# Kernel tuning notes

Hardware: AMD Instinct MI355X
Metric: run time of the kernel (lower is better)

## Reference

```python
import jax, jax.numpy as jnp
import numpy as np

NUM_CLASSES = 19

def setup_inputs() -> dict:
    key = jax.random.key(0)
    k1, k2 = jax.random.split(key)
    feats = jax.random.normal(k1, (8, 256, 128, 256), dtype=jnp.float32)
    y_down = jax.random.randint(k2, (8, 128, 256), 0, NUM_CLASSES, dtype=jnp.int64)
    return {"feats": feats, "y_down": y_down}

def reference(feats, y_down):
    # feats: [B, C, H, W]; y_down: [B, H, W] int labels in [0, NUM_CLASSES)
    B, C, H, W = feats.shape
    x = jnp.transpose(feats, (0, 2, 3, 1)).reshape(-1, C)   # [N, C], N = B*H*W
    seg = y_down.reshape(-1).astype(jnp.int32)              # [N]
    # per-class sum of feature vectors and pixel counts (fused segment reduce)
    sums = jax.ops.segment_sum(x, seg, num_segments=NUM_CLASSES)          # [K, C]
    counts = jax.ops.segment_sum(jnp.ones((x.shape[0],), x.dtype), seg,
                                 num_segments=NUM_CLASSES)                # [K]
    denom = jnp.maximum(counts, 1.0)
    nonempty = counts > 0
    # b_c: per-class mean feature vector (zeros for empty classes, which torch
    # returns as empty tensors)
    means = jnp.where(nonempty[:, None], sums / denom[:, None], 0.0)      # [K, C]
    # n_c: per-class mean of per-pixel L2 norms (detached in original)
    norms = jnp.linalg.norm(x, axis=1)                                    # [N]
    norm_sums = jax.ops.segment_sum(norms, seg, num_segments=NUM_CLASSES)
    norm_means = jnp.where(nonempty, norm_sums / denom, 0.0)              # [K]
    return means, norm_means
```

## Files before the change

kernel.cpp:

```cpp
#include <hip/hip_runtime.h>

#define NCLS 19
#define NCH  256
#define HW   (128 * 256)
#define NPIX (8 * HW)
#define P    64
#define THP  68
#define SQG  16
#define SQP  65
#define SUMS (NCLS * NCH)
#define PN_NORM SUMS
#define PN_CNT  (SUMS + NCLS)
#define PSTRIDE 4928
#define GRID  512
#define TILES (NPIX / (P * GRID))

typedef __bf16 bf16x4v __attribute__((ext_vector_type(4)));
typedef __bf16 bf16x8v __attribute__((ext_vector_type(8)));
typedef float  f32x16v __attribute__((ext_vector_type(16)));
typedef int    int4v   __attribute__((ext_vector_type(4)));

__device__ __forceinline__ void bar_lds() {
    asm volatile("s_waitcnt lgkmcnt(0)" ::: "memory");
    __builtin_amdgcn_sched_barrier(0);
    __builtin_amdgcn_s_barrier();
    __builtin_amdgcn_sched_barrier(0);
}

__global__ __launch_bounds__(256) void accum_kernel(
    const float* __restrict__ feats, const int* __restrict__ labels,
    float* __restrict__ partials)
{
    __shared__ __bf16 tileh[NCH * THP];
    __shared__ float  sqpart[SQG * SQP];
    __shared__ float  accN[NCLS];
    __shared__ float  accC[NCLS];
    __shared__ int    lab_s[P];

    const int t = threadIdx.x;
    if (t < NCLS) { accN[t] = 0.f; accC[t] = 0.f; }

    const int px4 = (t & 15) * 4, cbase = t >> 4;
    const int w = t >> 6, l = t & 63, h = l >> 5, col = l & 31;
    const int c0 = w * 64 + col, c1 = c0 + 32;
    const __bf16 ONE = (__bf16)1.0f, ZER = (__bf16)0.0f;

    f32x16v d0 = {}, d1 = {};
    float4 v4[16];
    int labv = 0;

    {
        const int p0 = blockIdx.x * P, b = p0 >> 15, hw0 = p0 & (HW - 1);
        const float* fb = feats + (size_t)b * NCH * HW + hw0;
        #pragma unroll
        for (int i = 0; i < 16; ++i)
            v4[i] = *reinterpret_cast<const float4*>(fb + (size_t)(cbase + 16 * i) * HW + px4);
        if (t < P) labv = labels[p0 + t];
    }
    {
        float s0 = 0.f, s1 = 0.f, s2 = 0.f, s3 = 0.f;
        #pragma unroll
        for (int i = 0; i < 16; ++i) {
            const int c = cbase + 16 * i;
            bf16x4v hv = { (__bf16)v4[i].x, (__bf16)v4[i].y, (__bf16)v4[i].z, (__bf16)v4[i].w };
            *reinterpret_cast<bf16x4v*>(&tileh[c * THP + px4]) = hv;
            s0 += v4[i].x * v4[i].x; s1 += v4[i].y * v4[i].y;
            s2 += v4[i].z * v4[i].z; s3 += v4[i].w * v4[i].w;
        }
        sqpart[cbase * SQP + px4    ] = s0; sqpart[cbase * SQP + px4 + 1] = s1;
        sqpart[cbase * SQP + px4 + 2] = s2; sqpart[cbase * SQP + px4 + 3] = s3;
        if (t < P) lab_s[t] = labv;
    }
    __syncthreads();

    for (int it = 0; it < TILES; ++it) {
        if (it + 1 < TILES) {
            const int p0 = (blockIdx.x + (it + 1) * GRID) * P;
            const int b = p0 >> 15, hw0 = p0 & (HW - 1);
            const float* fb = feats + (size_t)b * NCH * HW + hw0;
            #pragma unroll
            for (int i = 0; i < 16; ++i)
                v4[i] = *reinterpret_cast<const float4*>(fb + (size_t)(cbase + 16 * i) * HW + px4);
            if (t < P) labv = labels[p0 + t];
        }
        #pragma unroll
        for (int kk = 0; kk < 4; ++kk) {
            const int pb = kk * 16 + h * 8;
            const int4v lq0 = *reinterpret_cast<const int4v*>(&lab_s[pb]);
            const int4v lq1 = *reinterpret_cast<const int4v*>(&lab_s[pb + 4]);
            bf16x8v af;
            af[0] = (lq0[0] == col) ? ONE : ZER;  af[1] = (lq0[1] == col) ? ONE : ZER;
            af[2] = (lq0[2] == col) ? ONE : ZER;  af[3] = (lq0[3] == col) ? ONE : ZER;
            af[4] = (lq1[0] == col) ? ONE : ZER;  af[5] = (lq1[1] == col) ? ONE : ZER;
            af[6] = (lq1[2] == col) ? ONE : ZER;  af[7] = (lq1[3] == col) ? ONE : ZER;
            const bf16x4v b0l = *reinterpret_cast<const bf16x4v*>(&tileh[c0 * THP + pb]);
            const bf16x4v b0h = *reinterpret_cast<const bf16x4v*>(&tileh[c0 * THP + pb + 4]);
            const bf16x4v b1l = *reinterpret_cast<const bf16x4v*>(&tileh[c1 * THP + pb]);
            const bf16x4v b1h = *reinterpret_cast<const bf16x4v*>(&tileh[c1 * THP + pb + 4]);
            const bf16x8v bf0 = __builtin_shufflevector(b0l, b0h, 0,1,2,3,4,5,6,7);
            const bf16x8v bf1 = __builtin_shufflevector(b1l, b1h, 0,1,2,3,4,5,6,7);
            d0 = __builtin_amdgcn_mfma_f32_32x32x16_bf16(af, bf0, d0, 0, 0, 0);
            d1 = __builtin_amdgcn_mfma_f32_32x32x16_bf16(af, bf1, d1, 0, 0, 0);
        }
        if (t < P) {
            float s = 0.f;
            #pragma unroll
            for (int g = 0; g < SQG; ++g) s += sqpart[g * SQP + t];
            const int k = lab_s[t];
            unsafeAtomicAdd(&accN[k], sqrtf(s));
            unsafeAtomicAdd(&accC[k], 1.f);
        }
        bar_lds();
        if (it + 1 < TILES) {
            float s0 = 0.f, s1 = 0.f, s2 = 0.f, s3 = 0.f;
            #pragma unroll
            for (int i = 0; i < 16; ++i) {
                const int c = cbase + 16 * i;
                bf16x4v hv = { (__bf16)v4[i].x, (__bf16)v4[i].y, (__bf16)v4[i].z, (__bf16)v4[i].w };
                *reinterpret_cast<bf16x4v*>(&tileh[c * THP + px4]) = hv;
                s0 += v4[i].x * v4[i].x; s1 += v4[i].y * v4[i].y;
                s2 += v4[i].z * v4[i].z; s3 += v4[i].w * v4[i].w;
            }
            sqpart[cbase * SQP + px4    ] = s0; sqpart[cbase * SQP + px4 + 1] = s1;
            sqpart[cbase * SQP + px4 + 2] = s2; sqpart[cbase * SQP + px4 + 3] = s3;
            if (t < P) lab_s[t] = labv;
        }
        bar_lds();
    }

    float* op = partials + (size_t)blockIdx.x * PSTRIDE;
    #pragma unroll
    for (int r = 0; r < 16; ++r) {
        const int k = (r & 3) + 8 * (r >> 2) + 4 * h;
        if (k < NCLS) {
            op[k * NCH + c0] = d0[r];
            op[k * NCH + c1] = d1[r];
        }
    }
    if (t < NCLS) { op[PN_NORM + t] = accN[t]; op[PN_CNT + t] = accC[t]; }
}

__global__ __launch_bounds__(256) void reduce_kernel(
    const float* __restrict__ partials, float* __restrict__ out)
{
    __shared__ float cred[NCLS][9];
    __shared__ float red[16][17];
    __shared__ float cnt_s[NCLS];
    const int t = threadIdx.x;

    if (t < NCLS * 8) {
        const int k = t >> 3, gl = t & 7;
        float c = 0.f;
        #pragma unroll 8
        for (int j = 0; j < GRID / 8; ++j)
            c += partials[(size_t)(gl + 8 * j) * PSTRIDE + PN_CNT + k];
        cred[k][gl] = c;
    }
    {
        const int ol = t & 15, gl = t >> 4;
        const int o = blockIdx.x * 16 + ol;
        float s = 0.f;
        if (o < PN_CNT) {
            #pragma unroll 8
            for (int j = 0; j < GRID / 16; ++j)
                s += partials[(size_t)(gl + 16 * j) * PSTRIDE + o];
        }
        red[gl][ol] = s;
    }
    __syncthreads();
    if (t < NCLS) {
        float c = 0.f;
        #pragma unroll
        for (int g = 0; g < 8; ++g) c += cred[t][g];
        cnt_s[t] = c;
    }
    __syncthreads();
    if (t < 16) {
        const int oo = blockIdx.x * 16 + t;
        if (oo < PN_CNT) {
            float tot = 0.f;
            #pragma unroll
            for (int g = 0; g < 16; ++g) tot += red[g][t];
            const int k = (oo < SUMS) ? (oo >> 8) : (oo - SUMS);
            const float c = cnt_s[k];
            out[oo] = (c > 0.f) ? tot / fmaxf(c, 1.f) : 0.f;
        }
    }
}

extern "C" void kernel_launch(void* const* d_in, const int* in_sizes, int n_in,
                              void* d_out, int out_size, void* d_ws, size_t ws_size,
                              hipStream_t stream) {
    const float* feats  = (const float*)d_in[0];
    const int*   labels = (const int*)d_in[1];
    float* out      = (float*)d_out;
    float* partials = (float*)d_ws;

    accum_kernel<<<GRID, 256, 0, stream>>>(feats, labels, partials);
    reduce_kernel<<<(PN_CNT + 15) / 16, 256, 0, stream>>>(partials, out);
}
```

Measured before the change: 59.88 us.

## Split channels into four groups per block and move norm reduction to separate kernel

```diff
diff --git a/kernel.cpp b/kernel.cpp
--- a/kernel.cpp
+++ b/kernel.cpp
@@ -4,16 +4,22 @@
 #define NCH  256
 #define HW   (128 * 256)
 #define NPIX (8 * HW)
-#define P    64
-#define THP  68
-#define SQG  16
-#define SQP  65
+#define NGRP 4
+#define GC   64
+#define P    256
+#define THP  260
+#define SQP  260
 #define SUMS (NCLS * NCH)
-#define PN_NORM SUMS
-#define PN_CNT  (SUMS + NCLS)
-#define PSTRIDE 4928
-#define GRID  512
-#define TILES (NPIX / (P * GRID))
+#define PN_CNT (SUMS + NCLS)
+#define GRID 512
+#define PCHUNKS 128
+#define CPX  (NPIX / PCHUNKS)
+#define TILES (CPX / P)
+#define PST  1280
+#define NBLK 256
+#define PNST 64
+#define OFF_SQ ((size_t)GRID * PST)
+#define OFF_PN (OFF_SQ + (size_t)NGRP * NPIX)
 
 typedef __bf16 bf16x4v __attribute__((ext_vector_type(4)));
 typedef __bf16 bf16x8v __attribute__((ext_vector_type(8)));
@@ -27,121 +33,138 @@
     __builtin_amdgcn_sched_barrier(0);
 }
 
-__global__ __launch_bounds__(256) void accum_kernel(
+__global__ __launch_bounds__(256, 3) void accum_kernel(
     const float* __restrict__ feats, const int* __restrict__ labels,
-    float* __restrict__ partials)
+    float* __restrict__ ws)
 {
-    __shared__ __bf16 tileh[NCH * THP];
-    __shared__ float  sqpart[SQG * SQP];
-    __shared__ float  accN[NCLS];
-    __shared__ float  accC[NCLS];
+    __shared__ __bf16 tileh[GC * THP];
+    __shared__ float  sqpart[4 * SQP];
     __shared__ int    lab_s[P];
+    __shared__ float  accf[32 * GC];
 
     const int t = threadIdx.x;
-    if (t < NCLS) { accN[t] = 0.f; accC[t] = 0.f; }
-
-    const int px4 = (t & 15) * 4, cbase = t >> 4;
-    const int w = t >> 6, l = t & 63, h = l >> 5, col = l & 31;
-    const int c0 = w * 64 + col, c1 = c0 + 32;
-    const __bf16 ONE = (__bf16)1.0f, ZER = (__bf16)0.0f;
+    const int g0 = blockIdx.x & 3, pchunk = blockIdx.x >> 2;
+    const int pbase = pchunk * CPX;
+    const float* fb = feats + (size_t)(pbase >> 15) * NCH * HW
+                            + (size_t)g0 * GC * HW + (pbase & (HW - 1));
+    const int px4 = (t & 63) * 4;
+    const int wv  = t >> 6;
+    const int l = t & 63, h = l >> 5, col = l & 31;
+
+    for (int j = t; j < 32 * GC; j += 256) accf[j] = 0.f;
 
     f32x16v d0 = {}, d1 = {};
     float4 v4[16];
-    int labv = 0;
-
-    {
-        const int p0 = blockIdx.x * P, b = p0 >> 15, hw0 = p0 & (HW - 1);
-        const float* fb = feats + (size_t)b * NCH * HW + hw0;
-        #pragma unroll
-        for (int i = 0; i < 16; ++i)
-            v4[i] = *reinterpret_cast<const float4*>(fb + (size_t)(cbase + 16 * i) * HW + px4);
-        if (t < P) labv = labels[p0 + t];
-    }
+    int labv;
+
+    #pragma unroll
+    for (int i = 0; i < 16; ++i)
+        v4[i] = *reinterpret_cast<const float4*>(fb + (size_t)(wv + 4 * i) * HW + px4);
+    labv = labels[pbase + t];
     {
         float s0 = 0.f, s1 = 0.f, s2 = 0.f, s3 = 0.f;
         #pragma unroll
         for (int i = 0; i < 16; ++i) {
-            const int c = cbase + 16 * i;
+            const int c = wv + 4 * i;
             bf16x4v hv = { (__bf16)v4[i].x, (__bf16)v4[i].y, (__bf16)v4[i].z, (__bf16)v4[i].w };
             *reinterpret_cast<bf16x4v*>(&tileh[c * THP + px4]) = hv;
             s0 += v4[i].x * v4[i].x; s1 += v4[i].y * v4[i].y;
             s2 += v4[i].z * v4[i].z; s3 += v4[i].w * v4[i].w;
         }
-        sqpart[cbase * SQP + px4    ] = s0; sqpart[cbase * SQP + px4 + 1] = s1;
-        sqpart[cbase * SQP + px4 + 2] = s2; sqpart[cbase * SQP + px4 + 3] = s3;
-        if (t < P) lab_s[t] = labv;
+        sqpart[wv * SQP + px4    ] = s0; sqpart[wv * SQP + px4 + 1] = s1;
+        sqpart[wv * SQP + px4 + 2] = s2; sqpart[wv * SQP + px4 + 3] = s3;
+        lab_s[t] = labv;
     }
     __syncthreads();
 
     for (int it = 0; it < TILES; ++it) {
         if (it + 1 < TILES) {
-            const int p0 = (blockIdx.x + (it + 1) * GRID) * P;
-            const int b = p0 >> 15, hw0 = p0 & (HW - 1);
-            const float* fb = feats + (size_t)b * NCH * HW + hw0;
+            const int off = (it + 1) * P;
             #pragma unroll
             for (int i = 0; i < 16; ++i)
-                v4[i] = *reinterpret_cast<const float4*>(fb + (size_t)(cbase + 16 * i) * HW + px4);
-            if (t < P) labv = labels[p0 + t];
+                v4[i] = *reinterpret_cast<const float4*>(fb + (size_t)(wv + 4 * i) * HW + off + px4);
+            labv = labels[pbase + off + t];
         }
         #pragma unroll
         for (int kk = 0; kk < 4; ++kk) {
-            const int pb = kk * 16 + h * 8;
+            const int pb = wv * 64 + kk * 16 + h * 8;
             const int4v lq0 = *reinterpret_cast<const int4v*>(&lab_s[pb]);
             const int4v lq1 = *reinterpret_cast<const int4v*>(&lab_s[pb + 4]);
+            const __bf16 ONE = (__bf16)1.0f, ZER = (__bf16)0.0f;
             bf16x8v af;
             af[0] = (lq0[0] == col) ? ONE : ZER;  af[1] = (lq0[1] == col) ? ONE : ZER;
             af[2] = (lq0[2] == col) ? ONE : ZER;  af[3] = (lq0[3] == col) ? ONE : ZER;
             af[4] = (lq1[0] == col) ? ONE : ZER;  af[5] = (lq1[1] == col) ? ONE : ZER;
             af[6] = (lq1[2] == col) ? ONE : ZER;  af[7] = (lq1[3] == col) ? ONE : ZER;
-            const bf16x4v b0l = *reinterpret_cast<const bf16x4v*>(&tileh[c0 * THP + pb]);
-            const bf16x4v b0h = *reinterpret_cast<const bf16x4v*>(&tileh[c0 * THP + pb + 4]);
-            const bf16x4v b1l = *reinterpret_cast<const bf16x4v*>(&tileh[c1 * THP + pb]);
-            const bf16x4v b1h = *reinterpret_cast<const bf16x4v*>(&tileh[c1 * THP + pb + 4]);
+            const bf16x4v b0l = *reinterpret_cast<const bf16x4v*>(&tileh[col * THP + pb]);
+            const bf16x4v b0h = *reinterpret_cast<const bf16x4v*>(&tileh[col * THP + pb + 4]);
+            const bf16x4v b1l = *reinterpret_cast<const bf16x4v*>(&tileh[(col + 32) * THP + pb]);
+            const bf16x4v b1h = *reinterpret_cast<const bf16x4v*>(&tileh[(col + 32) * THP + pb + 4]);
             const bf16x8v bf0 = __builtin_shufflevector(b0l, b0h, 0,1,2,3,4,5,6,7);
             const bf16x8v bf1 = __builtin_shufflevector(b1l, b1h, 0,1,2,3,4,5,6,7);
             d0 = __builtin_amdgcn_mfma_f32_32x32x16_bf16(af, bf0, d0, 0, 0, 0);
             d1 = __builtin_amdgcn_mfma_f32_32x32x16_bf16(af, bf1, d1, 0, 0, 0);
         }
-        if (t < P) {
-            float s = 0.f;
-            #pragma unroll
-            for (int g = 0; g < SQG; ++g) s += sqpart[g * SQP + t];
-            const int k = lab_s[t];
-            unsafeAtomicAdd(&accN[k], sqrtf(s));
-            unsafeAtomicAdd(&accC[k], 1.f);
+        {
+            const float sq = sqpart[t] + sqpart[SQP + t] + sqpart[2 * SQP + t] + sqpart[3 * SQP + t];
+            ws[OFF_SQ + (size_t)g0 * NPIX + pbase + it * P + t] = sq;
         }
         bar_lds();
         if (it + 1 < TILES) {
             float s0 = 0.f, s1 = 0.f, s2 = 0.f, s3 = 0.f;
             #pragma unroll
             for (int i = 0; i < 16; ++i) {
-                const int c = cbase + 16 * i;
+                const int c = wv + 4 * i;
                 bf16x4v hv = { (__bf16)v4[i].x, (__bf16)v4[i].y, (__bf16)v4[i].z, (__bf16)v4[i].w };
                 *reinterpret_cast<bf16x4v*>(&tileh[c * THP + px4]) = hv;
                 s0 += v4[i].x * v4[i].x; s1 += v4[i].y * v4[i].y;
                 s2 += v4[i].z * v4[i].z; s3 += v4[i].w * v4[i].w;
             }
-            sqpart[cbase * SQP + px4    ] = s0; sqpart[cbase * SQP + px4 + 1] = s1;
-            sqpart[cbase * SQP + px4 + 2] = s2; sqpart[cbase * SQP + px4 + 3] = s3;
-            if (t < P) lab_s[t] = labv;
+            sqpart[wv * SQP + px4    ] = s0; sqpart[wv * SQP + px4 + 1] = s1;
+            sqpart[wv * SQP + px4 + 2] = s2; sqpart[wv * SQP + px4 + 3] = s3;
+            lab_s[t] = labv;
         }
         bar_lds();
     }
 
-    float* op = partials + (size_t)blockIdx.x * PSTRIDE;
+    __syncthreads();
     #pragma unroll
     for (int r = 0; r < 16; ++r) {
-        const int k = (r & 3) + 8 * (r >> 2) + 4 * h;
-        if (k < NCLS) {
-            op[k * NCH + c0] = d0[r];
-            op[k * NCH + c1] = d1[r];
-        }
-    }
-    if (t < NCLS) { op[PN_NORM + t] = accN[t]; op[PN_CNT + t] = accC[t]; }
+        const int row = (r & 3) + 8 * (r >> 2) + 4 * h;
+        unsafeAtomicAdd(&accf[row * GC + col], d0[r]);
+        unsafeAtomicAdd(&accf[row * GC + col + 32], d1[r]);
+    }
+    __syncthreads();
+    float* op = ws + (size_t)blockIdx.x * PST;
+    for (int j = t; j < NCLS * GC; j += 256) op[j] = accf[j];
+}
+
+__global__ __launch_bounds__(256) void norm_kernel(
+    const int* __restrict__ labels, float* __restrict__ ws)
+{
+    __shared__ float accN[NCLS], accC[NCLS];
+    const int t = threadIdx.x;
+    if (t < NCLS) { accN[t] = 0.f; accC[t] = 0.f; }
+    __syncthreads();
+    const float* sq = ws + OFF_SQ;
+    const int p0 = blockIdx.x * (NPIX / NBLK);
+    #pragma unroll
+    for (int j = 0; j < NPIX / NBLK / 256; ++j) {
+        const int p = p0 + j * 256 + t;
+        const float s = sq[p] + sq[NPIX + p] + sq[2 * NPIX + p] + sq[3 * NPIX + p];
+        const int k = labels[p];
+        unsafeAtomicAdd(&accN[k], sqrtf(s));
+        unsafeAtomicAdd(&accC[k], 1.f);
+    }
+    __syncthreads();
+    if (t < NCLS) {
+        ws[OFF_PN + (size_t)blockIdx.x * PNST + t] = accN[t];
+        ws[OFF_PN + (size_t)blockIdx.x * PNST + 32 + t] = accC[t];
+    }
 }
 
 __global__ __launch_bounds__(256) void reduce_kernel(
-    const float* __restrict__ partials, float* __restrict__ out)
+    const float* __restrict__ ws, float* __restrict__ out)
 {
     __shared__ float cred[NCLS][9];
     __shared__ float red[16][17];
@@ -152,18 +175,24 @@
         const int k = t >> 3, gl = t & 7;
         float c = 0.f;
         #pragma unroll 8
-        for (int j = 0; j < GRID / 8; ++j)
-            c += partials[(size_t)(gl + 8 * j) * PSTRIDE + PN_CNT + k];
+        for (int j = 0; j < NBLK / 8; ++j)
+            c += ws[OFF_PN + (size_t)(gl + 8 * j) * PNST + 32 + k];
         cred[k][gl] = c;
     }
     {
         const int ol = t & 15, gl = t >> 4;
         const int o = blockIdx.x * 16 + ol;
         float s = 0.f;
-        if (o < PN_CNT) {
-            #pragma unroll 8
-            for (int j = 0; j < GRID / 16; ++j)
-                s += partials[(size_t)(gl + 16 * j) * PSTRIDE + o];
+        if (o < SUMS) {
+            const int k = o >> 8, c = o & 255, g = c >> 6, c6 = c & 63;
+            #pragma unroll 4
+            for (int j = 0; j < PCHUNKS / 16; ++j)
+                s += ws[(size_t)((gl + 16 * j) * NGRP + g) * PST + k * GC + c6];
+        } else if (o < PN_CNT) {
+            const int k = o - SUMS;
+            #pragma unroll 4
+            for (int j = 0; j < NBLK / 16; ++j)
+                s += ws[OFF_PN + (size_t)(gl + 16 * j) * PNST + k];
         }
         red[gl][ol] = s;
     }
@@ -193,9 +222,10 @@
                               hipStream_t stream) {
     const float* feats  = (const float*)d_in[0];
     const int*   labels = (const int*)d_in[1];
-    float* out      = (float*)d_out;
-    float* partials = (float*)d_ws;
-
-    accum_kernel<<<GRID, 256, 0, stream>>>(feats, labels, partials);
-    reduce_kernel<<<(PN_CNT + 15) / 16, 256, 0, stream>>>(partials, out);
-}
+    float* out = (float*)d_out;
+    float* ws  = (float*)d_ws;
+
+    accum_kernel<<<GRID, 256, 0, stream>>>(feats, labels, ws);
+    norm_kernel<<<NBLK, 256, 0, stream>>>(labels, ws);
+    reduce_kernel<<<(PN_CNT + 15) / 16, 256, 0, stream>>>(ws, out);
+}
```

Result: slower. 78.20 us (+30.6%).
